# Optimization experiments

Measured on AMD Instinct MI355X. Metric: run time of the kernel, lower is better.

The kernel has to match this reference:

```python
import jax, jax.numpy as jnp
import numpy as np

D_MODEL = 2048
N_HEAD = 16
N_KV_HEAD = 4
D_HEAD = D_MODEL // N_HEAD  # 128
WINDOW = 512
B, T = 2, 2048


def _rope_tables(T, d_head, base=10000.0):
    inv = 1.0 / (base ** (np.arange(0, d_head, 2, dtype=np.float32) / d_head))
    t = np.arange(T, dtype=np.float32)
    freqs = np.outer(t, inv)  # [T, d_head//2]
    return jnp.asarray(np.cos(freqs)), jnp.asarray(np.sin(freqs))


def setup_inputs() -> dict:
    key = jax.random.key(0)
    ks = jax.random.split(key, 5)
    cos, sin = _rope_tables(T, D_HEAD)
    s = 1.0 / np.sqrt(D_MODEL)
    return {
        "x": jax.random.normal(ks[0], (B, T, D_MODEL), jnp.float32),
        "cos": cos,
        "sin": sin,
        "Wq": jax.random.normal(ks[1], (D_MODEL, D_MODEL), jnp.float32) * s,
        "Wk": jax.random.normal(ks[2], (D_MODEL, N_KV_HEAD * D_HEAD), jnp.float32) * s,
        "Wv": jax.random.normal(ks[3], (D_MODEL, N_KV_HEAD * D_HEAD), jnp.float32) * s,
        "Wo": jax.random.normal(ks[4], (D_MODEL, D_MODEL), jnp.float32) * s,
    }


def _apply_rope(t, cos, sin):
    # t: [B, T, H, D]; cos/sin: [T, D//2]; interleaved-pair (complex) rotation
    tr = t[..., 0::2]
    ti = t[..., 1::2]
    c = cos[None, :, None, :]
    s = sin[None, :, None, :]
    out_r = tr * c - ti * s
    out_i = tr * s + ti * c
    return jnp.stack([out_r, out_i], axis=-1).reshape(t.shape)


def reference(x, cos, sin, Wq, Wk, Wv, Wo):
    Bx, Tx, C = x.shape
    q = (x @ Wq).reshape(Bx, Tx, N_HEAD, D_HEAD)       # [B,T,H,D]
    k = (x @ Wk).reshape(Bx, Tx, N_KV_HEAD, D_HEAD)    # [B,T,Hkv,D]
    v = (x @ Wv).reshape(Bx, Tx, N_KV_HEAD, D_HEAD)
    q = _apply_rope(q, cos, sin)
    k = _apply_rope(k, cos, sin)
    n_rep = N_HEAD // N_KV_HEAD
    k = jnp.repeat(k, n_rep, axis=2)  # [B,T,H,D]
    v = jnp.repeat(v, n_rep, axis=2)
    scale = 1.0 / np.sqrt(D_HEAD)
    att = jnp.einsum("bihd,bjhd->bhij", q, k) * scale  # [B,H,T,T]
    i = jnp.arange(Tx)[:, None]
    j = jnp.arange(Tx)[None, :]
    mask = (j <= i) & (j >= i - WINDOW + 1)            # causal sliding window
    att = jnp.where(mask[None, None], att, -jnp.inf)
    att = jax.nn.softmax(att, axis=-1)
    y = jnp.einsum("bhij,bjhd->bihd", att, v).reshape(Bx, Tx, C)
    return y @ Wo
```

## Files before the change

### kernel.cpp

```cpp
#include <hip/hip_runtime.h>
#include <hip/hip_bf16.h>
#include <cstdint>
#include <cstddef>

#define B_ 2
#define T_ 2048
#define NH 16
#define NKV 4
#define DH 128
#define DM 2048
#define WIN 512
#define QKS 2560

typedef __attribute__((ext_vector_type(4))) float f32x4;
typedef __attribute__((ext_vector_type(8))) __bf16 bf16x8;

using bf16 = __hip_bfloat16;

__device__ inline void gload_lds16(const void* g, void* l) {
  __builtin_amdgcn_global_load_lds(
      (const __attribute__((address_space(1))) void*)g,
      (__attribute__((address_space(3))) void*)l, 16, 0, 0);
}

__device__ inline unsigned pack_bf2(float a, float b) {
  unsigned short ua = __builtin_bit_cast(unsigned short, __float2bfloat16(a));
  unsigned short ub = __builtin_bit_cast(unsigned short, __float2bfloat16(b));
  return (unsigned)ua | ((unsigned)ub << 16);
}

#define FBAR()                           \
  do {                                   \
    asm volatile("" ::: "memory");       \
    __builtin_amdgcn_s_barrier();        \
    asm volatile("" ::: "memory");       \
  } while (0)

__global__ __launch_bounds__(256) void k_prep(const float* __restrict__ x,
                                              const float* __restrict__ Wq,
                                              const float* __restrict__ Wk,
                                              const float* __restrict__ Wv,
                                              const float* __restrict__ Wo,
                                              bf16* __restrict__ xb,
                                              bf16* __restrict__ Wqkvt,
                                              bf16* __restrict__ Wot) {
  int id = blockIdx.x;
  int tid = threadIdx.x;
  if (id >= 2560) {
    size_t base = (size_t)(id - 2560) * 4096 + tid * 16;
#pragma unroll
    for (int j = 0; j < 4; ++j) {
      float4 v = *(const float4*)(x + base + j * 4);
      ushort4 o;
      o.x = __builtin_bit_cast(unsigned short, __float2bfloat16(v.x));
      o.y = __builtin_bit_cast(unsigned short, __float2bfloat16(v.y));
      o.z = __builtin_bit_cast(unsigned short, __float2bfloat16(v.z));
      o.w = __builtin_bit_cast(unsigned short, __float2bfloat16(v.w));
      *(ushort4*)(xb + base + j * 4) = o;
    }
    return;
  }
  const float* W;
  bf16* Wt;
  int N, bx, by;
  if (id < 1024) { W = Wq; Wt = Wqkvt; N = 2048; bx = id & 31; by = id >> 5; }
  else if (id < 1280) { id -= 1024; W = Wk; Wt = Wqkvt + (size_t)2048 * 2048; N = 512; bx = id & 7; by = id >> 3; }
  else if (id < 1536) { id -= 1280; W = Wv; Wt = Wqkvt + (size_t)2560 * 2048; N = 512; bx = id & 7; by = id >> 3; }
  else { id -= 1536; W = Wo; Wt = Wot; N = 2048; bx = id & 31; by = id >> 5; }

  __shared__ float tile[64][65];
  int n0 = bx * 64, k0 = by * 64;
  int tx = tid & 63, tg = tid >> 6;
#pragma unroll
  for (int r = 0; r < 16; ++r) {
    int k = tg * 16 + r;
    tile[k][tx] = W[(size_t)(k0 + k) * N + n0 + tx];
  }
  __syncthreads();
#pragma unroll
  for (int r = 0; r < 16; ++r) {
    int nn = tg * 16 + r;
    Wt[(size_t)(n0 + nn) * 2048 + k0 + tx] = __float2bfloat16(tile[tx][nn]);
  }
}

template <int BN, int EPI>
__global__ __launch_bounds__(512, 4) void k_gemm1(const bf16* __restrict__ A,
                                                  const bf16* __restrict__ Bt,
                                                  void* __restrict__ Cout,
                                                  int M, int N, int K,
                                                  const float* __restrict__ cosT,
                                                  const float* __restrict__ sinT,
                                                  bf16* __restrict__ vt) {
  constexpr int NR = BN / 64;
  constexpr int NB = BN * 128 / 8192;
  __shared__ __align__(16) char As_[2][16384];
  __shared__ __align__(16) char Bs_[2][BN * 128];

  const int tid = threadIdx.x;
  const int w = tid >> 6, lane = tid & 63;
  const int li = lane & 15, g = lane >> 4;
  const int wm = w >> 2, wn = w & 3;

  const int nwg = gridDim.x * gridDim.y;
  int bid = blockIdx.y * gridDim.x + blockIdx.x;
  bid = (bid & 7) * (nwg >> 3) + (bid >> 3);
  const int m0 = (bid / gridDim.x) * 128;
  const int n0 = (bid % gridDim.x) * BN;

  const int ntiles = K >> 6;

  auto sA = [&](int buf, int tile, int h) {
    if (tile >= ntiles) return;
    const int rl = tid >> 3;
    const int row = (rl & 31) + h * 32 + ((rl >> 5) << 6);
    const int sl = tid & 7;
    const bf16* src = A + (size_t)(m0 + row) * K + tile * 64 + ((sl ^ (rl & 7)) * 8);
    gload_lds16(src, As_[buf] + h * 8192 + tid * 16);
  };
  auto sB = [&](int buf, int tile, int issue) {
    if (tile >= ntiles) return;
    const int block = issue * 8 + w;
    const int rr = block * 8 + (lane >> 3);
    const int sl = lane & 7;
    const bf16* src = Bt + (size_t)(n0 + rr) * K + tile * 64 + ((sl ^ (rr & 7)) * 8);
    gload_lds16(src, Bs_[buf] + block * 1024);
  };

  const int swz0 = (g ^ (li & 7)) * 16;
  const int swz1 = ((4 + g) ^ (li & 7)) * 16;
  bf16x8 af[8], bv[NR * 2];
  f32x4 acc[4][NR] = {};

  auto readA = [&](int buf) {
#pragma unroll
    for (int mf = 0; mf < 4; ++mf) {
      const int h = (mf >> 1) & 1;
      const int rl = (mf & 1) * 16 + li + 32 * wm;
      const char* p = As_[buf] + h * 8192 + rl * 128;
      af[mf * 2 + 0] = *(const bf16x8*)(p + swz0);
      af[mf * 2 + 1] = *(const bf16x8*)(p + swz1);
    }
  };
  auto readB = [&](int buf) {
#pragma unroll
    for (int n = 0; n < NR; ++n) {
      const char* p = Bs_[buf] + (wn * (NR * 16) + n * 16 + li) * 128;
      bv[n * 2 + 0] = *(const bf16x8*)(p + swz0);
      bv[n * 2 + 1] = *(const bf16x8*)(p + swz1);
    }
  };
  auto MMA = [&]() {
    __builtin_amdgcn_s_setprio(1);
#pragma unroll
    for (int mf = 0; mf < 4; ++mf)
#pragma unroll
      for (int n = 0; n < NR; ++n)
#pragma unroll
        for (int kk = 0; kk < 2; ++kk)
          acc[mf][n] = __builtin_amdgcn_mfma_f32_16x16x32_bf16(
              af[mf * 2 + kk], bv[n * 2 + kk], acc[mf][n], 0, 0, 0);
    __builtin_amdgcn_s_setprio(0);
  };

  sA(0, 0, 0); sA(0, 0, 1);
#pragma unroll
  for (int i = 0; i < NB; ++i) sB(0, 0, i);

  for (int t = 0; t < ntiles; ++t) {
    const int cb = t & 1;
    const bool last = (t == ntiles - 1);
    sA(cb ^ 1, t + 1, 0); sA(cb ^ 1, t + 1, 1);
#pragma unroll
    for (int i = 0; i < NB; ++i) sB(cb ^ 1, t + 1, i);
    if (last)
      asm volatile("s_waitcnt vmcnt(0)" ::: "memory");
    else if constexpr (NB == 3)
      asm volatile("s_waitcnt vmcnt(5)" ::: "memory");
    else
      asm volatile("s_waitcnt vmcnt(4)" ::: "memory");
    __builtin_amdgcn_sched_barrier(0);
    FBAR();
    readA(cb); readB(cb);
    MMA();
    FBAR();
  }

#pragma unroll
  for (int mf = 0; mf < 4; ++mf)
#pragma unroll
    for (int nf = 0; nf < NR; ++nf) {
      const int colc = n0 + wn * (NR * 16) + nf * 16;
      const int col = colc + li;
      const int row0 = m0 + wm * 64 + mf * 16 + g * 4;
      if constexpr (EPI == 2) {
        if (colc < QKS) {
          const float qs = (colc < 2048) ? 0.08838834764831845f : 1.0f;
          const int i = (col & 127) >> 1;
          const float sgn = (li & 1) ? 1.0f : -1.0f;
#pragma unroll
          for (int r = 0; r < 4; ++r) {
            const int trow = (row0 + r) & (T_ - 1);
            float v = acc[mf][nf][r];
            float pv = __shfl_xor(v, 1);
            float c = cosT[trow * 64 + i], s = sinT[trow * 64 + i];
            float o = (v * c + pv * (sgn * s)) * qs;
            ((bf16*)Cout)[(size_t)(row0 + r) * QKS + col] = __float2bfloat16(o);
          }
        } else {
          unsigned lo = pack_bf2(acc[mf][nf][0], acc[mf][nf][1]);
          unsigned hi = pack_bf2(acc[mf][nf][2], acc[mf][nf][3]);
          uint2 pk = {lo, hi};
          *(uint2*)(vt + (size_t)(col - QKS) * (B_ * T_) + row0) = pk;
        }
      } else {
#pragma unroll
        for (int r = 0; r < 4; ++r)
          ((float*)Cout)[(size_t)(row0 + r) * N + col] = acc[mf][nf][r];
      }
    }
}

__global__ __launch_bounds__(512) void k_attn(const bf16* __restrict__ qkv,
                                              const bf16* __restrict__ vt,
                                              bf16* __restrict__ Y) {
  __shared__ __align__(16) char Ks[2][9216];
  __shared__ __align__(16) char Vs[2][10240];
  __shared__ __align__(16) char Pl[8][1280];
  const int lane = threadIdx.x & 63;
  const int w = threadIdx.x >> 6;
  const int li = lane & 15, g = lane >> 4;
  const int t0 = ((int)gridDim.x - 1 - (int)blockIdx.x) * 32;
  const int b = blockIdx.y / NKV, kvh = blockIdx.y % NKV;
  const int h = kvh * 4 + (w >> 1);
  const int qrow0 = t0 + (w & 1) * 16;
  const int t = qrow0 + li;

  bf16x8 qf[4];
  const bf16* qbase = qkv + (size_t)(b * T_ + qrow0 + li) * QKS + h * DH;
#pragma unroll
  for (int dk = 0; dk < 4; ++dk) qf[dk] = *(const bf16x8*)(qbase + dk * 32 + g * 8);

  float mrow = -1e4f;
  float srow = 0.f;
  f32x4 acc[8] = {};

  int ks0 = t0 - (WIN - 1);
  if (ks0 < 0) ks0 = 0;
  ks0 &= ~31;
  const int nt = (t0 + 31 - ks0) / 32 + 1;

  const bf16* kgbase = qkv + (size_t)(b * T_) * QKS + DM + kvh * DH;
  const bf16* vgbase = vt + (size_t)(kvh * DH) * (B_ * T_) + b * T_;

  auto STAGE = [&](int buf, int kt) {
    for (int c = w; c < 19; c += 8) {
      if (c < 9) {
        int slot = c * 64 + lane;
        int row = slot / 17, cc = slot % 17;
        if (slot >= 544) { row = 0; cc = 0; }
        if (cc == 16) cc = 0;
        const bf16* src = kgbase + (size_t)(kt + row) * QKS + cc * 8;
        gload_lds16(src, Ks[buf] + c * 1024);
      } else {
        int c2 = c - 9;
        int slot = c2 * 64 + lane;
        int row = slot / 5, cc = slot % 5;
        if (cc == 4) cc = 0;
        const bf16* src = vgbase + (size_t)row * (B_ * T_) + kt + cc * 8;
        gload_lds16(src, Vs[buf] + c2 * 1024);
      }
    }
  };

  STAGE(0, ks0);
  __syncthreads();
  int cur = 0;

  for (int it = 0; it < nt; ++it) {
    const int kt = ks0 + it * 32;
    if (it + 1 < nt) STAGE(cur ^ 1, kt + 32);

    f32x4 sc[2] = {};
#pragma unroll
    for (int n = 0; n < 2; ++n)
#pragma unroll
      for (int dk = 0; dk < 4; ++dk) {
        bf16x8 kf = *(const bf16x8*)(Ks[cur] + (n * 16 + li) * 272 + dk * 64 + g * 16);
        sc[n] = __builtin_amdgcn_mfma_f32_16x16x32_bf16(kf, qf[dk], sc[n], 0, 0, 0);
      }

    float p[2][4];
    float pmax = -1e30f;
#pragma unroll
    for (int n = 0; n < 2; ++n)
#pragma unroll
      for (int r = 0; r < 4; ++r) {
        int key = kt + n * 16 + g * 4 + r;
        bool valid = (key <= t) && (key > t - WIN);
        float pv = valid ? sc[n][r] : -1e30f;
        p[n][r] = pv;
        pmax = fmaxf(pmax, pv);
      }
    pmax = fmaxf(pmax, __shfl_xor(pmax, 16));
    pmax = fmaxf(pmax, __shfl_xor(pmax, 32));

    if (!__all(pmax <= mrow)) {
      float nm = fmaxf(mrow, pmax);
      float alpha = __expf(mrow - nm);
      mrow = nm;
      srow *= alpha;
      float af_[4];
#pragma unroll
      for (int r = 0; r < 4; ++r) af_[r] = __shfl(alpha, (g << 2) + r);
#pragma unroll
      for (int db = 0; db < 8; ++db)
#pragma unroll
        for (int r = 0; r < 4; ++r) acc[db][r] *= af_[r];
    }

    float rs = 0.f;
#pragma unroll
    for (int n = 0; n < 2; ++n)
#pragma unroll
      for (int r = 0; r < 4; ++r) {
        p[n][r] = __expf(p[n][r] - mrow);
        rs += p[n][r];
      }
    rs += __shfl_xor(rs, 16);
    rs += __shfl_xor(rs, 32);
    srow += rs;

#pragma unroll
    for (int n = 0; n < 2; ++n) {
      *(unsigned*)(Pl[w] + li * 80 + n * 32 + g * 8) = pack_bf2(p[n][0], p[n][1]);
      *(unsigned*)(Pl[w] + li * 80 + n * 32 + g * 8 + 4) = pack_bf2(p[n][2], p[n][3]);
    }

    bf16x8 pf = *(const bf16x8*)(Pl[w] + li * 80 + g * 16);
#pragma unroll
    for (int db = 0; db < 8; ++db) {
      bf16x8 vf = *(const bf16x8*)(Vs[cur] + (db * 16 + li) * 80 + g * 16);
      acc[db] = __builtin_amdgcn_mfma_f32_16x16x32_bf16(pf, vf, acc[db], 0, 0, 0);
    }

    __syncthreads();
    cur ^= 1;
  }

  float inv[4];
#pragma unroll
  for (int r = 0; r < 4; ++r) inv[r] = 1.f / __shfl(srow, (g << 2) + r);
  bf16* ybase = Y + (size_t)(b * T_ + qrow0 + (g << 2)) * DM + h * DH;
#pragma unroll
  for (int r = 0; r < 4; ++r)
#pragma unroll
    for (int db = 0; db < 8; ++db)
      ybase[(size_t)r * DM + db * 16 + li] = __float2bfloat16(acc[db][r] * inv[r]);
}

extern "C" void kernel_launch(void* const* d_in, const int* in_sizes, int n_in,
                              void* d_out, int out_size, void* d_ws, size_t ws_size,
                              hipStream_t stream) {
  const float* x = (const float*)d_in[0];
  const float* cosT = (const float*)d_in[1];
  const float* sinT = (const float*)d_in[2];
  const float* Wq = (const float*)d_in[3];
  const float* Wk = (const float*)d_in[4];
  const float* Wv = (const float*)d_in[5];
  const float* Wo = (const float*)d_in[6];
  float* out = (float*)d_out;

  char* ws = (char*)d_ws;
  bf16* xb = (bf16*)ws;     ws += (size_t)4096 * 2048 * 2;
  bf16* Wqkvt = (bf16*)ws;  ws += (size_t)3072 * 2048 * 2;
  bf16* Wot = (bf16*)ws;    ws += (size_t)2048 * 2048 * 2;
  bf16* qkv = (bf16*)ws;    ws += (size_t)4096 * QKS * 2;
  bf16* vt = (bf16*)ws;     ws += (size_t)512 * 4096 * 2;
  bf16* yb = xb;

  k_prep<<<4608, 256, 0, stream>>>(x, Wq, Wk, Wv, Wo, xb, Wqkvt, Wot);

  k_gemm1<192, 2><<<dim3(3072 / 192, 4096 / 128), 512, 0, stream>>>(
      xb, Wqkvt, qkv, 4096, 3072, 2048, cosT, sinT, vt);

  k_attn<<<dim3(T_ / 32, B_ * NKV), 512, 0, stream>>>(qkv, vt, yb);

  k_gemm1<128, 0><<<dim3(2048 / 128, 4096 / 128), 512, 0, stream>>>(
      yb, Wot, out, 4096, 2048, 2048, nullptr, nullptr, nullptr);
}
```

Before: 155.0 us.

## Load GEMM A-operand directly into registers, bypassing LDS, with register double-buffering

The GEMM kernel no longer stages the A tile through shared memory. Each wave loads its A fragments straight from global memory into registers, double-buffered across two register sets, while B still goes through LDS with async global-to-LDS loads. The QKV projection also moves from a 192-wide to a 128-wide N tile. This cuts LDS traffic and LDS capacity use, but each wave now issues uncoalesced 16-byte global loads for A, and A rows are re-read by every wave column, which adds global/L2 traffic and register pressure.

```diff
diff --git a/kernel.cpp b/kernel.cpp
--- a/kernel.cpp
+++ b/kernel.cpp
@@ -84,18 +84,17 @@
   }
 }
 
-template <int BN, int EPI>
-__global__ __launch_bounds__(512, 4) void k_gemm1(const bf16* __restrict__ A,
-                                                  const bf16* __restrict__ Bt,
-                                                  void* __restrict__ Cout,
-                                                  int M, int N, int K,
-                                                  const float* __restrict__ cosT,
-                                                  const float* __restrict__ sinT,
-                                                  bf16* __restrict__ vt) {
-  constexpr int NR = BN / 64;
-  constexpr int NB = BN * 128 / 8192;
-  __shared__ __align__(16) char As_[2][16384];
-  __shared__ __align__(16) char Bs_[2][BN * 128];
+template <int EPI>
+__global__ __launch_bounds__(512, 4) void k_gA(const bf16* __restrict__ A,
+                                               const bf16* __restrict__ Bt,
+                                               void* __restrict__ Cout,
+                                               int M, int N, int K,
+                                               const float* __restrict__ cosT,
+                                               const float* __restrict__ sinT,
+                                               bf16* __restrict__ vt) {
+  constexpr int NR = 2;
+  constexpr int NB = 2;
+  __shared__ __align__(16) char Bs_[2][16384];
 
   const int tid = threadIdx.x;
   const int w = tid >> 6, lane = tid & 63;
@@ -106,20 +105,12 @@
   int bid = blockIdx.y * gridDim.x + blockIdx.x;
   bid = (bid & 7) * (nwg >> 3) + (bid >> 3);
   const int m0 = (bid / gridDim.x) * 128;
-  const int n0 = (bid % gridDim.x) * BN;
+  const int n0 = (bid % gridDim.x) * 128;
 
   const int ntiles = K >> 6;
-
-  auto sA = [&](int buf, int tile, int h) {
-    if (tile >= ntiles) return;
-    const int rl = tid >> 3;
-    const int row = (rl & 31) + h * 32 + ((rl >> 5) << 6);
-    const int sl = tid & 7;
-    const bf16* src = A + (size_t)(m0 + row) * K + tile * 64 + ((sl ^ (rl & 7)) * 8);
-    gload_lds16(src, As_[buf] + h * 8192 + tid * 16);
-  };
+  const int NT2 = ntiles >> 1;
+
   auto sB = [&](int buf, int tile, int issue) {
-    if (tile >= ntiles) return;
     const int block = issue * 8 + w;
     const int rr = block * 8 + (lane >> 3);
     const int sl = lane & 7;
@@ -129,18 +120,18 @@
 
   const int swz0 = (g ^ (li & 7)) * 16;
   const int swz1 = ((4 + g) ^ (li & 7)) * 16;
-  bf16x8 af[8], bv[NR * 2];
+  bf16x8 afA[8], afB[8], bv[NR * 2];
   f32x4 acc[4][NR] = {};
 
-  auto readA = [&](int buf) {
-#pragma unroll
-    for (int mf = 0; mf < 4; ++mf) {
-      const int h = (mf >> 1) & 1;
-      const int rl = (mf & 1) * 16 + li + 32 * wm;
-      const char* p = As_[buf] + h * 8192 + rl * 128;
-      af[mf * 2 + 0] = *(const bf16x8*)(p + swz0);
-      af[mf * 2 + 1] = *(const bf16x8*)(p + swz1);
-    }
+  const bf16* aBase = A + (size_t)(m0 + wm * 64 + li) * K + g * 8;
+
+  auto loadA = [&](bf16x8* af, int tile) {
+#pragma unroll
+    for (int mf = 0; mf < 4; ++mf)
+#pragma unroll
+      for (int kk = 0; kk < 2; ++kk)
+        af[mf * 2 + kk] =
+            *(const bf16x8*)(aBase + (size_t)(mf * 16) * K + tile * 64 + kk * 32);
   };
   auto readB = [&](int buf) {
 #pragma unroll
@@ -150,7 +141,7 @@
       bv[n * 2 + 1] = *(const bf16x8*)(p + swz1);
     }
   };
-  auto MMA = [&]() {
+  auto MMA = [&](const bf16x8* af) {
     __builtin_amdgcn_s_setprio(1);
 #pragma unroll
     for (int mf = 0; mf < 4; ++mf)
@@ -163,27 +154,44 @@
     __builtin_amdgcn_s_setprio(0);
   };
 
-  sA(0, 0, 0); sA(0, 0, 1);
-#pragma unroll
-  for (int i = 0; i < NB; ++i) sB(0, 0, i);
-
-  for (int t = 0; t < ntiles; ++t) {
-    const int cb = t & 1;
-    const bool last = (t == ntiles - 1);
-    sA(cb ^ 1, t + 1, 0); sA(cb ^ 1, t + 1, 1);
-#pragma unroll
-    for (int i = 0; i < NB; ++i) sB(cb ^ 1, t + 1, i);
-    if (last)
-      asm volatile("s_waitcnt vmcnt(0)" ::: "memory");
-    else if constexpr (NB == 3)
-      asm volatile("s_waitcnt vmcnt(5)" ::: "memory");
-    else
-      asm volatile("s_waitcnt vmcnt(4)" ::: "memory");
-    __builtin_amdgcn_sched_barrier(0);
-    FBAR();
-    readA(cb); readB(cb);
-    MMA();
-    FBAR();
+  loadA(afA, 0);
+  sB(0, 0, 0); sB(0, 0, 1);
+
+  for (int itr = 0; itr < NT2; ++itr) {
+    {
+      const int t = itr * 2;
+      const bool more = (t + 1 < ntiles);
+      if (more) {
+        loadA(afB, t + 1);
+        sB(1, t + 1, 0); sB(1, t + 1, 1);
+      }
+      if (more)
+        asm volatile("s_waitcnt vmcnt(10)" ::: "memory");
+      else
+        asm volatile("s_waitcnt vmcnt(0)" ::: "memory");
+      __builtin_amdgcn_sched_barrier(0);
+      FBAR();
+      readB(0);
+      MMA(afA);
+      FBAR();
+    }
+    {
+      const int t = itr * 2 + 1;
+      const bool more = (t + 1 < ntiles);
+      if (more) {
+        loadA(afA, t + 1);
+        sB(0, t + 1, 0); sB(0, t + 1, 1);
+      }
+      if (more)
+        asm volatile("s_waitcnt vmcnt(10)" ::: "memory");
+      else
+        asm volatile("s_waitcnt vmcnt(0)" ::: "memory");
+      __builtin_amdgcn_sched_barrier(0);
+      FBAR();
+      readB(1);
+      MMA(afB);
+      FBAR();
+    }
   }
 
 #pragma unroll
@@ -381,11 +389,11 @@
 
   k_prep<<<4608, 256, 0, stream>>>(x, Wq, Wk, Wv, Wo, xb, Wqkvt, Wot);
 
-  k_gemm1<192, 2><<<dim3(3072 / 192, 4096 / 128), 512, 0, stream>>>(
+  k_gA<2><<<dim3(3072 / 128, 4096 / 128), 512, 0, stream>>>(
       xb, Wqkvt, qkv, 4096, 3072, 2048, cosT, sinT, vt);
 
   k_attn<<<dim3(T_ / 32, B_ * NKV), 512, 0, stream>>>(qkv, vt, yb);
 
-  k_gemm1<128, 0><<<dim3(2048 / 128, 4096 / 128), 512, 0, stream>>>(
+  k_gA<0><<<dim3(2048 / 128, 4096 / 128), 512, 0, stream>>>(
       yb, Wot, out, 4096, 2048, 2048, nullptr, nullptr, nullptr);
 }
```

Result: slower. 380.2 us (+145.3%).
